# Optimization experiments

Hardware: AMD Instinct MI355X
Metric: run time of the kernel (lower is better)

## Reference

```python
import jax, jax.numpy as jnp
import numpy as np

B, C, H, W = 64, 2048, 24, 8
NUM_IDS = 751


def setup_inputs() -> dict:
    key = jax.random.key(0)
    k1, k2, k3 = jax.random.split(key, 3)
    features_map = jax.random.normal(k1, (B, C, H, W), dtype=jnp.float32)
    classifier_weight = jax.random.normal(k2, (NUM_IDS, C), dtype=jnp.float32) * 0.02
    pids = jax.random.randint(k3, (B,), 0, NUM_IDS, dtype=jnp.int64)
    return {"features_map": features_map, "classifier_weight": classifier_weight, "pids": pids}


def reference(features_map, classifier_weight, pids):
    b, c, h, w = features_map.shape
    # gather one classifier weight row per sample: [B, C]
    wrows = classifier_weight[pids]
    # per-sample 1xC @ Cx(H*W) matmul -> heatmap [B, H, W]
    heat = jnp.einsum('bc,bchw->bhw', wrows, features_map)
    hflat = heat.reshape(b, h * w)
    mn = hflat.min(axis=-1, keepdims=True)
    mx = hflat.max(axis=-1, keepdims=True)
    # original: normalize only if max != 0
    hflat = jnp.where(mx != 0, (hflat - mn) / (mx - mn), hflat)
    heat = jax.lax.stop_gradient(hflat.reshape(b, h, w))  # heatmap is detached
    return features_map * heat[:, None, :, :]
```

## Files before the change

kernel.cpp:

```cpp
#include <hip/hip_runtime.h>

#define BB 64
#define CC 2048
#define HWN 192
#define HW4 48
#define NCHUNK 16
#define CCHUNK 128
#define TPB 384
#define CLANES 8

typedef float f32x4 __attribute__((ext_vector_type(4)));

#define PART_OFF  0
#define HEATN_OFF (BB * NCHUNK * HWN)

__global__ void __launch_bounds__(TPB) heat_partial_kernel(
    const float* __restrict__ f,
    const float* __restrict__ w,
    const int* __restrict__ pids,
    float* __restrict__ ws)
{
    float* partial = ws + PART_OFF;

    const int blk = blockIdx.x;
    const int b = blk >> 4;
    const int k = blk & (NCHUNK - 1);
    const int tid = threadIdx.x;
    const int hw4 = tid % HW4;
    const int cl  = tid / HW4;

    __shared__ float wsm[CCHUNK];
    __shared__ __align__(16) float4 red[TPB];

    const int row = pids[b];
    if (tid < CCHUNK) wsm[tid] = w[(size_t)row * CC + (size_t)k * CCHUNK + tid];
    __syncthreads();

    const size_t base = ((size_t)b * CC + (size_t)k * CCHUNK) * HW4;
    const float4* fb4 = (const float4*)f + base;

    float4 acc = make_float4(0.f, 0.f, 0.f, 0.f);
#pragma unroll
    for (int i = 0; i < CCHUNK / CLANES; ++i) {
        float4 v = fb4[(size_t)i * TPB + tid];
        float wv = wsm[cl + i * CLANES];
        acc.x = fmaf(wv, v.x, acc.x);
        acc.y = fmaf(wv, v.y, acc.y);
        acc.z = fmaf(wv, v.z, acc.z);
        acc.w = fmaf(wv, v.w, acc.w);
    }
    red[tid] = acc;
    __syncthreads();
    if (tid < HW4) {
        float4 s = red[tid];
#pragma unroll
        for (int j = 1; j < CLANES; ++j) {
            float4 a = red[tid + j * HW4];
            s.x += a.x; s.y += a.y; s.z += a.z; s.w += a.w;
        }
        ((float4*)partial)[(size_t)(b * NCHUNK + k) * HW4 + tid] = s;
    }
}

__global__ void __launch_bounds__(HWN) normalize_kernel(
    float* __restrict__ ws)
{
    const float* partial = ws + PART_OFF;
    float* heatN = ws + HEATN_OFF;

    const int b = blockIdx.x;
    const int tid = threadIdx.x;

    __shared__ float vals[HWN];
    __shared__ float s_mn, s_mx;

    const float* pb = partial + (size_t)b * NCHUNK * HWN + tid;
    float v = 0.f;
#pragma unroll
    for (int kk = 0; kk < NCHUNK; ++kk) v += pb[kk * HWN];
    vals[tid] = v;
    __syncthreads();

    if (tid < 64) {
        float m0 = vals[tid], m1 = vals[tid + 64], m2 = vals[tid + 128];
        float mn = fminf(m0, fminf(m1, m2));
        float mx = fmaxf(m0, fmaxf(m1, m2));
        for (int off = 32; off > 0; off >>= 1) {
            mn = fminf(mn, __shfl_down(mn, off));
            mx = fmaxf(mx, __shfl_down(mx, off));
        }
        if (tid == 0) { s_mn = mn; s_mx = mx; }
    }
    __syncthreads();

    const float mn = s_mn, mx = s_mx;
    heatN[(size_t)b * HWN + tid] = (mx != 0.f) ? (v - mn) / (mx - mn) : v;
}

__global__ void __launch_bounds__(TPB) scale_kernel(
    const float* __restrict__ f,
    const float* __restrict__ ws,
    float* __restrict__ out)
{
    const float* heatN = ws + HEATN_OFF;
    const int blk = blockIdx.x;
    const int b = blk >> 4;
    const int k = blk & (NCHUNK - 1);
    const int tid = threadIdx.x;
    const int hw4 = tid % HW4;

    const f32x4 hv = ((const f32x4*)(heatN + (size_t)b * HWN))[hw4];

    const size_t base = ((size_t)b * CC + (size_t)k * CCHUNK) * HW4;
    const f32x4* fb4 = (const f32x4*)f + base;
    f32x4* ob4 = (f32x4*)out + base;

#pragma unroll
    for (int i = 0; i < (CCHUNK * HW4) / TPB; ++i) {
        const size_t idx = (size_t)i * TPB + tid;
        f32x4 x = fb4[idx];
        x *= hv;
        __builtin_nontemporal_store(x, &ob4[idx]);
    }
}

extern "C" void kernel_launch(void* const* d_in, const int* in_sizes, int n_in,
                              void* d_out, int out_size, void* d_ws, size_t ws_size,
                              hipStream_t stream) {
    const float* features = (const float*)d_in[0];
    const float* weight   = (const float*)d_in[1];
    const int*   pids     = (const int*)d_in[2];
    float* out = (float*)d_out;
    float* ws  = (float*)d_ws;

    heat_partial_kernel<<<BB * NCHUNK, TPB, 0, stream>>>(features, weight, pids, ws);
    normalize_kernel<<<BB, HWN, 0, stream>>>(ws);
    scale_kernel<<<BB * NCHUNK, TPB, 0, stream>>>(features, ws, out);
}
```

Measured before the change: 197.4 us.

## Fuse heat, normalize and scale kernels with per-sample atomic counter barrier

After: 309.5 us. 1.57x slower.

```diff
diff --git a/kernel.cpp b/kernel.cpp
--- a/kernel.cpp
+++ b/kernel.cpp
@@ -11,16 +11,18 @@
 
 typedef float f32x4 __attribute__((ext_vector_type(4)));
 
-#define PART_OFF  0
-#define HEATN_OFF (BB * NCHUNK * HWN)
+#define PART_OFF 0
+#define CNT_OFF  (BB * NCHUNK * HWN)
 
-__global__ void __launch_bounds__(TPB) heat_partial_kernel(
+__global__ void __launch_bounds__(TPB, 6) fused_kernel(
     const float* __restrict__ f,
     const float* __restrict__ w,
     const int* __restrict__ pids,
+    float* __restrict__ out,
     float* __restrict__ ws)
 {
     float* partial = ws + PART_OFF;
+    int*   cnt     = (int*)(ws + CNT_OFF);
 
     const int blk = blockIdx.x;
     const int b = blk >> 4;
@@ -30,57 +32,49 @@
     const int cl  = tid / HW4;
 
     __shared__ float wsm[CCHUNK];
-    __shared__ __align__(16) float4 red[TPB];
+    __shared__ __align__(16) f32x4 red[TPB];
+    __shared__ __align__(16) float hl[HWN];
+    __shared__ float s_mn, s_mx;
 
     const int row = pids[b];
     if (tid < CCHUNK) wsm[tid] = w[(size_t)row * CC + (size_t)k * CCHUNK + tid];
     __syncthreads();
 
     const size_t base = ((size_t)b * CC + (size_t)k * CCHUNK) * HW4;
-    const float4* fb4 = (const float4*)f + base;
+    const f32x4* fb4 = (const f32x4*)f + base;
 
-    float4 acc = make_float4(0.f, 0.f, 0.f, 0.f);
+    f32x4 acc = (f32x4)(0.f);
 #pragma unroll
     for (int i = 0; i < CCHUNK / CLANES; ++i) {
-        float4 v = fb4[(size_t)i * TPB + tid];
-        float wv = wsm[cl + i * CLANES];
-        acc.x = fmaf(wv, v.x, acc.x);
-        acc.y = fmaf(wv, v.y, acc.y);
-        acc.z = fmaf(wv, v.z, acc.z);
-        acc.w = fmaf(wv, v.w, acc.w);
+        f32x4 v = fb4[(size_t)i * TPB + tid];
+        acc += wsm[cl + i * CLANES] * v;
     }
     red[tid] = acc;
     __syncthreads();
     if (tid < HW4) {
-        float4 s = red[tid];
+        f32x4 s = red[tid];
 #pragma unroll
-        for (int j = 1; j < CLANES; ++j) {
-            float4 a = red[tid + j * HW4];
-            s.x += a.x; s.y += a.y; s.z += a.z; s.w += a.w;
-        }
-        ((float4*)partial)[(size_t)(b * NCHUNK + k) * HW4 + tid] = s;
+        for (int j = 1; j < CLANES; ++j) s += red[tid + j * HW4];
+        ((f32x4*)partial)[(size_t)(b * NCHUNK + k) * HW4 + tid] = s;
     }
-}
-
-__global__ void __launch_bounds__(HWN) normalize_kernel(
-    float* __restrict__ ws)
-{
-    const float* partial = ws + PART_OFF;
-    float* heatN = ws + HEATN_OFF;
-
-    const int b = blockIdx.x;
-    const int tid = threadIdx.x;
-
-    __shared__ float vals[HWN];
-    __shared__ float s_mn, s_mx;
-
-    const float* pb = partial + (size_t)b * NCHUNK * HWN + tid;
-    float v = 0.f;
-#pragma unroll
-    for (int kk = 0; kk < NCHUNK; ++kk) v += pb[kk * HWN];
-    vals[tid] = v;
+    if (tid == 0) {
+        __threadfence();
+        __hip_atomic_fetch_add(&cnt[b], 1, __ATOMIC_ACQ_REL, __HIP_MEMORY_SCOPE_AGENT);
+        while (__hip_atomic_load(&cnt[b], __ATOMIC_RELAXED, __HIP_MEMORY_SCOPE_AGENT) < NCHUNK)
+            __builtin_amdgcn_s_sleep(2);
+        __threadfence();
+    }
     __syncthreads();
 
+    float v = 0.f;
+    if (tid < HWN) {
+        const float* pb = partial + (size_t)b * NCHUNK * HWN + tid;
+#pragma unroll
+        for (int kk = 0; kk < NCHUNK; ++kk) v += pb[kk * HWN];
+    }
+    float* vals = (float*)red;
+    if (tid < HWN) vals[tid] = v;
+    __syncthreads();
     if (tid < 64) {
         float m0 = vals[tid], m1 = vals[tid + 64], m2 = vals[tid + 128];
         float mn = fminf(m0, fminf(m1, m2));
@@ -92,29 +86,14 @@
         if (tid == 0) { s_mn = mn; s_mx = mx; }
     }
     __syncthreads();
+    if (tid < HWN) {
+        const float mn = s_mn, mx = s_mx;
+        hl[tid] = (mx != 0.f) ? (v - mn) / (mx - mn) : v;
+    }
+    __syncthreads();
 
-    const float mn = s_mn, mx = s_mx;
-    heatN[(size_t)b * HWN + tid] = (mx != 0.f) ? (v - mn) / (mx - mn) : v;
-}
-
-__global__ void __launch_bounds__(TPB) scale_kernel(
-    const float* __restrict__ f,
-    const float* __restrict__ ws,
-    float* __restrict__ out)
-{
-    const float* heatN = ws + HEATN_OFF;
-    const int blk = blockIdx.x;
-    const int b = blk >> 4;
-    const int k = blk & (NCHUNK - 1);
-    const int tid = threadIdx.x;
-    const int hw4 = tid % HW4;
-
-    const f32x4 hv = ((const f32x4*)(heatN + (size_t)b * HWN))[hw4];
-
-    const size_t base = ((size_t)b * CC + (size_t)k * CCHUNK) * HW4;
-    const f32x4* fb4 = (const f32x4*)f + base;
+    const f32x4 hv = ((const f32x4*)hl)[hw4];
     f32x4* ob4 = (f32x4*)out + base;
-
 #pragma unroll
     for (int i = 0; i < (CCHUNK * HW4) / TPB; ++i) {
         const size_t idx = (size_t)i * TPB + tid;
@@ -133,7 +112,7 @@
     float* out = (float*)d_out;
     float* ws  = (float*)d_ws;
 
-    heat_partial_kernel<<<BB * NCHUNK, TPB, 0, stream>>>(features, weight, pids, ws);
-    normalize_kernel<<<BB, HWN, 0, stream>>>(ws);
-    scale_kernel<<<BB * NCHUNK, TPB, 0, stream>>>(features, ws, out);
+    hipMemsetAsync((char*)d_ws + CNT_OFF * sizeof(float), 0, BB * sizeof(int), stream);
+
+    fused_kernel<<<BB * NCHUNK, TPB, 0, stream>>>(features, weight, pids, out, ws);
 }
```
